# Kernel optimization log

Measured on AMD Instinct MI355X. Metric: run time of the kernel, lower is better.

## Reference

```python
import jax, jax.numpy as jnp
import numpy as np

E, H, I, R, T, TOPK = 8, 1024, 2816, 8, 4096, 2
SCALING = 2.0  # lora_alpha / r = 16 / 8


def setup_inputs() -> dict:
    key = jax.random.key(0)
    ks = jax.random.split(key, 12)
    inp = {
        "hidden_states": jax.random.normal(ks[0], (T, H), dtype=jnp.float32),
        "routing_weights": jax.random.uniform(ks[1], (T, TOPK), dtype=jnp.float32),
        "selected_experts": jax.random.randint(ks[2], (T, TOPK), 0, E),
        # frozen base expert weights, (G, K, N) layout
        "gate_proj": jax.random.normal(ks[3], (E, H, I), dtype=jnp.float32) * 0.02,
        "up_proj": jax.random.normal(ks[4], (E, H, I), dtype=jnp.float32) * 0.02,
        "down_proj": jax.random.normal(ks[5], (E, I, H), dtype=jnp.float32) * 0.02,
        # LoRA adapters, A: [E, in, r], B: [E, r, out]  (B random, not zero, so delta is exercised)
        "gate_A": jax.random.normal(ks[6], (E, H, R), dtype=jnp.float32) * 0.02,
        "gate_B": jax.random.normal(ks[7], (E, R, I), dtype=jnp.float32) * 0.02,
        "up_A": jax.random.normal(ks[8], (E, H, R), dtype=jnp.float32) * 0.02,
        "up_B": jax.random.normal(ks[9], (E, R, I), dtype=jnp.float32) * 0.02,
        "down_A": jax.random.normal(ks[10], (E, I, R), dtype=jnp.float32) * 0.02,
        "down_B": jax.random.normal(ks[11], (E, R, H), dtype=jnp.float32) * 0.02,
    }
    return inp


def _moe_lora_forward(x, routing_weights, selected_experts,
                      gate_proj, up_proj, down_proj,
                      gate_A, gate_B, up_A, up_B, down_A, down_B):
    # combine weights per (token, expert): [T, E]
    combine = jnp.sum(
        jax.nn.one_hot(selected_experts, E, dtype=x.dtype) * routing_weights[..., None],
        axis=1,
    )
    out = jnp.zeros_like(x)
    for e in range(E):  # static small loop over experts
        g = x @ gate_proj[e] + SCALING * ((x @ gate_A[e]) @ gate_B[e])
        u = x @ up_proj[e] + SCALING * ((x @ up_A[e]) @ up_B[e])
        h = jax.nn.silu(g) * u  # [T, I]
        y = h @ down_proj[e] + SCALING * ((h @ down_A[e]) @ down_B[e])  # [T, H]
        out = out + combine[:, e:e + 1] * y
    return out


def reference(hidden_states, routing_weights, selected_experts,
              gate_proj, up_proj, down_proj,
              gate_A, gate_B, up_A, up_B, down_A, down_B):
    return _moe_lora_forward(hidden_states, routing_weights, selected_experts,
                             gate_proj, up_proj, down_proj,
                             gate_A, gate_B, up_A, up_B, down_A, down_B)
```

## Files before the change

kernel.cpp:

```cpp
#include <hip/hip_runtime.h>
#include <stdint.h>

#define T_TOK 4096
#define NE 8
#define HH 1024
#define II 2816
#define HE 1056
#define IEW 2944
#define HT 23
#define RRK 8
#define NPAIR (T_TOK*2)
#define ROWCAP 10240
#define MT_MAX 40
#define SCAL 2.0f

typedef short v8s __attribute__((ext_vector_type(8)));
typedef float v4f __attribute__((ext_vector_type(4)));

__device__ __forceinline__ unsigned short f2bf(float f){
  union { float f; unsigned u; } c; c.f = f;
  unsigned u = c.u;
  u += 0x7FFFu + ((u >> 16) & 1u);
  return (unsigned short)(u >> 16);
}
__device__ __forceinline__ float bf2f(unsigned short h){
  union { unsigned u; float f; } c; c.u = ((unsigned)h) << 16;
  return c.f;
}
__device__ __forceinline__ void gload16(const void* g, void* l){
  __builtin_amdgcn_global_load_lds(
      (const __attribute__((address_space(1))) unsigned int*)g,
      (__attribute__((address_space(3))) unsigned int*)l, 16, 0, 0);
}
__device__ __forceinline__ void fence_(){ asm volatile("" ::: "memory"); }

__global__ void route_count(const int* __restrict__ sel, int* __restrict__ counts,
                            int* __restrict__ bases, int* __restrict__ tile_e,
                            int* __restrict__ tile_r0){
  __shared__ int c[NE];
  int tid = threadIdx.x;
  if (tid < NE) c[tid] = 0;
  __syncthreads();
  for (int p = tid; p < NPAIR; p += 256) atomicAdd(&c[sel[p]], 1);
  __syncthreads();
  if (tid == 0){
    int b = 0;
    for (int e = 0; e < NE; e++){ counts[e] = c[e]; bases[e] = b; b += ((c[e] + 255) >> 8) << 8; }
    bases[NE] = b;
    int t = 0;
    for (int e = 0; e < NE; e++){
      int nt = (c[e] + 255) >> 8;
      for (int i = 0; i < nt; i++){ tile_e[t] = e; tile_r0[t] = bases[e] + i * 256; t++; }
    }
    for (; t < MT_MAX; t++){ tile_e[t] = -1; tile_r0[t] = 0; }
  }
}

__global__ void route_fill(const int* __restrict__ sel, const float* __restrict__ rw,
                           const int* __restrict__ bases,
                           int* __restrict__ row_token, int* __restrict__ row_expert,
                           float* __restrict__ row_w, int* __restrict__ pair2row){
  int e = blockIdx.x;
  int lane = threadIdx.x;
  if (e == NE){
    for (int idx = bases[NE] + lane; idx < ROWCAP; idx += 64){
      row_token[idx] = -1; row_expert[idx] = 0; row_w[idx] = 0.f;
    }
    return;
  }
  int base = bases[e];
  int cnt = 0;
  for (int chunk = 0; chunk < NPAIR; chunk += 64){
    int p = chunk + lane;
    bool m = (sel[p] == e);
    unsigned long long mask = __ballot(m);
    if (m){
      int pos = __popcll(mask & ((1ull << lane) - 1ull));
      int dst = base + cnt + pos;
      row_token[dst] = p >> 1;
      row_expert[dst] = e;
      row_w[dst] = rw[p];
      pair2row[p] = dst;
    }
    cnt += __popcll(mask);
  }
  int nb = bases[e + 1];
  for (int idx = base + cnt + lane; idx < nb; idx += 64){
    row_token[idx] = -1; row_expert[idx] = e; row_w[idx] = 0.f;
  }
}

__global__ void transpose_cvt(const float* __restrict__ W, unsigned short* __restrict__ Wt,
                              int K, int N, int KE){
  int e = blockIdx.y;
  int tilesK = K >> 6;
  int kt = (blockIdx.x % tilesK) * 64;
  int nt = (blockIdx.x / tilesK) * 64;
  __shared__ float tile[64][65];
  int tid = threadIdx.x;
  int r = tid >> 2;
  int c0 = (tid & 3) * 16;
  const float* src = W + (size_t)e * K * N + (size_t)(kt + r) * N + nt + c0;
  #pragma unroll
  for (int i = 0; i < 4; i++){
    float4 v = *(const float4*)(src + i * 4);
    tile[r][c0 + i*4 + 0] = v.x; tile[r][c0 + i*4 + 1] = v.y;
    tile[r][c0 + i*4 + 2] = v.z; tile[r][c0 + i*4 + 3] = v.w;
  }
  __syncthreads();
  union { unsigned short us[16]; uint4 q[2]; } pk;
  #pragma unroll
  for (int j = 0; j < 16; j++) pk.us[j] = f2bf(tile[c0 + j][r]);
  unsigned short* dst = Wt + (size_t)e * N * KE + (size_t)(nt + r) * KE + kt + c0;
  *(uint4*)(dst) = pk.q[0];
  *(uint4*)(dst + 8) = pk.q[1];
}

__global__ void ext_fill_pair(unsigned short* __restrict__ Wtg, unsigned short* __restrict__ Wtu,
                              const float* __restrict__ gB, const float* __restrict__ uB){
  int idx = blockIdx.x * 256 + threadIdx.x;
  if (idx >= NE * II) return;
  int e = idx / II, n = idx % II;
  unsigned short* g = Wtg + ((size_t)e * II + n) * HE + HH;
  unsigned short* u = Wtu + ((size_t)e * II + n) * HE + HH;
  #pragma unroll
  for (int j = 0; j < 8; j++){
    g[j] = f2bf(gB[((size_t)e * RRK + j) * II + n]);
    u[j] = 0;
    g[8 + j] = 0;
    u[8 + j] = f2bf(uB[((size_t)e * RRK + j) * II + n]);
  }
  #pragma unroll
  for (int j = 16; j < 32; j++){ g[j] = 0; u[j] = 0; }
}

__global__ void ext_fill_down(unsigned short* __restrict__ Wtd, const float* __restrict__ dB){
  int idx = blockIdx.x * 256 + threadIdx.x;
  if (idx >= NE * HH) return;
  int e = idx / HH, n = idx % HH;
  unsigned short* d = Wtd + ((size_t)e * HH + n) * IEW + II;
  #pragma unroll
  for (int j = 0; j < 8; j++) d[j] = f2bf(dB[((size_t)e * RRK + j) * HH + n]);
  for (int j = 8; j < 128; j++) d[j] = 0;
}

__global__ void gxa_kernel(const float* __restrict__ x, const float* __restrict__ gA,
                           const float* __restrict__ uA, const int* __restrict__ row_token,
                           const int* __restrict__ row_expert,
                           unsigned short* __restrict__ Xg){
  int p = blockIdx.x; int tid = threadIdx.x;
  int tok = row_token[p]; int e = row_expert[p];
  int k0 = tid * 4;
  float4 xv = make_float4(0.f, 0.f, 0.f, 0.f);
  if (tok >= 0) xv = *(const float4*)(x + (size_t)tok * HH + k0);
  uint2 o;
  o.x = (unsigned)f2bf(xv.x) | ((unsigned)f2bf(xv.y) << 16);
  o.y = (unsigned)f2bf(xv.z) | ((unsigned)f2bf(xv.w) << 16);
  *(uint2*)(Xg + (size_t)p * HE + k0) = o;

  float ag[8], au[8];
  #pragma unroll
  for (int r = 0; r < 8; r++){ ag[r] = 0.f; au[r] = 0.f; }
  if (tok >= 0){
    const float* pg = gA + ((size_t)e * HH + k0) * RRK;
    const float* pu = uA + ((size_t)e * HH + k0) * RRK;
    float xs[4] = {xv.x, xv.y, xv.z, xv.w};
    #pragma unroll
    for (int j = 0; j < 4; j++){
      #pragma unroll
      for (int r = 0; r < 8; r++){
        ag[r] += xs[j] * pg[j * RRK + r];
        au[r] += xs[j] * pu[j * RRK + r];
      }
    }
  }
  __shared__ float redg[8][4], redu[8][4];
  int lane = tid & 63, wv = tid >> 6;
  #pragma unroll
  for (int r = 0; r < 8; r++){
    float v1 = ag[r], v2 = au[r];
    for (int off = 32; off > 0; off >>= 1){ v1 += __shfl_down(v1, off); v2 += __shfl_down(v2, off); }
    if (lane == 0){ redg[r][wv] = v1; redu[r][wv] = v2; }
  }
  __syncthreads();
  if (tid < 8)
    Xg[(size_t)p * HE + HH + tid] = f2bf(SCAL * (redg[tid][0] + redg[tid][1] + redg[tid][2] + redg[tid][3]));
  else if (tid < 16){
    int r = tid - 8;
    Xg[(size_t)p * HE + HH + 8 + r] = f2bf(SCAL * (redu[r][0] + redu[r][1] + redu[r][2] + redu[r][3]));
  } else if (tid < 32){
    Xg[(size_t)p * HE + HH + tid] = 0;
  }
}

__global__ void ha_kernel(const unsigned short* __restrict__ hbuf, const float* __restrict__ dA,
                          const int* __restrict__ row_expert, unsigned short* __restrict__ hout){
  int p = blockIdx.x; int tid = threadIdx.x;
  int e = row_expert[p];
  float a[8];
  #pragma unroll
  for (int r = 0; r < 8; r++) a[r] = 0.f;
  for (int i = 0; i < 11; i++){
    int k = i * 256 + tid;
    float hv = bf2f(hbuf[(size_t)(k >> 7) * (ROWCAP * 128) + (size_t)p * 128 + (k & 127)]);
    const float* pd = dA + ((size_t)e * II + k) * RRK;
    #pragma unroll
    for (int r = 0; r < 8; r++) a[r] += hv * pd[r];
  }
  __shared__ float red[8][4];
  int lane = tid & 63, wv = tid >> 6;
  #pragma unroll
  for (int r = 0; r < 8; r++){
    float v = a[r];
    for (int off = 32; off > 0; off >>= 1) v += __shfl_down(v, off);
    if (lane == 0) red[r][wv] = v;
  }
  __syncthreads();
  unsigned short* ext = hout + (size_t)22 * (ROWCAP * 128) + (size_t)p * 128;
  if (tid < 8)
    ext[tid] = f2bf(SCAL * (red[tid][0] + red[tid][1] + red[tid][2] + red[tid][3]));
  else if (tid < 128)
    ext[tid] = 0;
}

__launch_bounds__(512, 2)
__global__ void gemm1_kernel(const unsigned short* __restrict__ Xg,
                             const unsigned short* __restrict__ Wtg,
                             const unsigned short* __restrict__ Wtu,
                             const int* __restrict__ tile_e,
                             const int* __restrict__ tile_r0,
                             unsigned short* __restrict__ hbuf){
  int hw = blockIdx.x;
  int lg = (hw & 7) * 110 + (hw >> 3);
  int mt = lg / 22;
  int n0 = (lg % 22) * 128;

  int e = tile_e[mt];
  if (e < 0) return;
  int row0 = tile_r0[mt];

  __shared__ unsigned short lds[2][4 * 4096];
  int tid = threadIdx.x;
  int lane = tid & 63;
  int w = tid >> 6;
  int wm = w >> 1;
  int wn = w & 1;
  int g = lane >> 4, r16 = lane & 15;

  const unsigned short* srcA = Xg + (size_t)row0 * HE;
  const unsigned short* srcG = Wtg + ((size_t)e * II + n0) * HE;
  const unsigned short* srcU = Wtu + ((size_t)e * II + n0) * HE;

  v4f accg[4][4], accu[4][4];
  #pragma unroll
  for (int i = 0; i < 4; i++)
    #pragma unroll
    for (int j = 0; j < 4; j++){
      accg[i][j] = (v4f){0.f, 0.f, 0.f, 0.f};
      accu[i][j] = (v4f){0.f, 0.f, 0.f, 0.f};
    }

  int uA0 = tid, uA1 = tid + 512;
  int rA0 = uA0 >> 2, rA1 = uA1 >> 2;
  size_t gA0 = (size_t)rA0 * HE + ((uA0 & 3) ^ ((rA0 >> 1) & 3)) * 8;
  size_t gA1 = (size_t)rA1 * HE + ((uA1 & 3) ^ ((rA1 >> 1) & 3)) * 8;
  int lA0 = (uA0 & ~63) * 8, lA1 = (uA1 & ~63) * 8;
  int rB = tid >> 2;
  size_t gB = (size_t)rB * HE + ((tid & 3) ^ ((rB >> 1) & 3)) * 8;
  int lB = (tid & ~63) * 8;

  const int NT = HE / 32;

  {
    unsigned short* buf = lds[0];
    gload16(srcA + gA0, buf + lA0);
    gload16(srcA + gA1, buf + lA1);
    gload16(srcG + gB, buf + 8192 + lB);
    gload16(srcU + gB, buf + 12288 + lB);
  }

  for (int t = 0; t < NT; t++){
    if (t + 1 < NT){
      unsigned short* nbuf = lds[(t + 1) & 1];
      int ks = (t + 1) * 32;
      gload16(srcA + gA0 + ks, nbuf + lA0);
      gload16(srcA + gA1 + ks, nbuf + lA1);
      gload16(srcG + gB + ks, nbuf + 8192 + lB);
      gload16(srcU + gB + ks, nbuf + 12288 + lB);
      asm volatile("s_waitcnt vmcnt(4)" ::: "memory");
    } else {
      asm volatile("s_waitcnt vmcnt(0)" ::: "memory");
    }
    __builtin_amdgcn_s_barrier();
    fence_();
    const unsigned short* buf = lds[t & 1];
    v8s a[4], bg[4], bu[4];
    #pragma unroll
    for (int f = 0; f < 4; f++){
      int rowA = wm * 64 + f * 16 + r16;
      int ca = g ^ ((rowA >> 1) & 3);
      a[f] = *(const v8s*)(buf + rowA * 32 + ca * 8);
      int rowB = wn * 64 + f * 16 + r16;
      int cb = g ^ ((rowB >> 1) & 3);
      bg[f] = *(const v8s*)(buf + 8192 + rowB * 32 + cb * 8);
      bu[f] = *(const v8s*)(buf + 12288 + rowB * 32 + cb * 8);
    }
    #pragma unroll
    for (int fm = 0; fm < 4; fm++)
      #pragma unroll
      for (int fn = 0; fn < 4; fn++){
        accg[fm][fn] = __builtin_amdgcn_mfma_f32_16x16x32_bf16(a[fm], bg[fn], accg[fm][fn], 0, 0, 0);
        accu[fm][fn] = __builtin_amdgcn_mfma_f32_16x16x32_bf16(a[fm], bu[fn], accu[fm][fn], 0, 0, 0);
      }
    fence_();
    __builtin_amdgcn_s_barrier();
    fence_();
  }

  unsigned short* sh = (unsigned short*)lds;
  #pragma unroll
  for (int fm = 0; fm < 4; fm++)
    #pragma unroll
    for (int fn = 0; fn < 4; fn++)
      #pragma unroll
      for (int r = 0; r < 4; r++){
        int lrow = wm * 64 + fm * 16 + g * 4 + r;
        int lcol = wn * 64 + fn * 16 + r16;
        float gg = accg[fm][fn][r];
        float uu = accu[fm][fn][r];
        float hh = (gg / (1.f + __expf(-gg))) * uu;
        int ch = (lcol >> 3) ^ (lrow & 7);
        sh[lrow * 128 + ch * 8 + (lcol & 7)] = f2bf(hh);
      }
  __syncthreads();
  unsigned short* dst = hbuf + ((size_t)(n0 >> 7) * ROWCAP + row0) * 128;
  #pragma unroll
  for (int pass = 0; pass < 8; pass++){
    int idx2 = pass * 512 + tid;
    int row = idx2 >> 4;
    int ch = idx2 & 15;
    int chs = ch ^ (row & 7);
    v8s val = *(const v8s*)(sh + row * 128 + chs * 8);
    *(v8s*)(dst + row * 128 + ch * 8) = val;
  }
}

__launch_bounds__(512, 2)
__global__ void gemm2_kernel(const unsigned short* __restrict__ hbuf,
                             const unsigned short* __restrict__ Wtd,
                             const int* __restrict__ tile_e,
                             const int* __restrict__ tile_r0,
                             const float* __restrict__ row_w,
                             float* __restrict__ Y){
  int hw = blockIdx.x;
  int lg = (hw & 7) * 20 + (hw >> 3);
  int mt = lg / 4;
  int n0 = (lg % 4) * 256;

  int e = tile_e[mt];
  if (e < 0) return;
  int row0 = tile_r0[mt];

  __shared__ unsigned short lds[2][2 * 8192];
  int tid = threadIdx.x;
  int lane = tid & 63;
  int w = tid >> 6;
  int wm = w >> 1;
  int wn = w & 1;
  int g = lane >> 4, r16 = lane & 15;

  const unsigned short* srcA = hbuf + (size_t)row0 * 128;
  const unsigned short* srcB = Wtd + ((size_t)e * HH + n0) * IEW;

  v4f acc[4][8];
  #pragma unroll
  for (int i = 0; i < 4; i++)
    #pragma unroll
    for (int j = 0; j < 8; j++) acc[i][j] = (v4f){0.f, 0.f, 0.f, 0.f};

  int u0 = tid, u1 = tid + 512;
  int r0_ = u0 >> 2, r1_ = u1 >> 2;
  int c0_ = (u0 & 3) ^ ((r0_ >> 1) & 3), c1_ = (u1 & 3) ^ ((r1_ >> 1) & 3);
  size_t aoff0 = (size_t)r0_ * 128 + c0_ * 8;
  size_t aoff1 = (size_t)r1_ * 128 + c1_ * 8;
  size_t boff0 = (size_t)r0_ * IEW + c0_ * 8;
  size_t boff1 = (size_t)r1_ * IEW + c1_ * 8;
  int l0 = (u0 & ~63) * 8, l1 = (u1 & ~63) * 8;

  const int NT = IEW / 32;

  {
    unsigned short* buf = lds[0];
    gload16(srcA + aoff0, buf + l0);
    gload16(srcA + aoff1, buf + l1);
    gload16(srcB + boff0, buf + 8192 + l0);
    gload16(srcB + boff1, buf + 8192 + l1);
  }

  for (int t = 0; t < NT; t++){
    if (t + 1 < NT){
      unsigned short* nbuf = lds[(t + 1) & 1];
      int ks = (t + 1) * 32;
      size_t abase = (size_t)(ks >> 7) * (ROWCAP * 128) + (ks & 127);
      gload16(srcA + abase + aoff0, nbuf + l0);
      gload16(srcA + abase + aoff1, nbuf + l1);
      gload16(srcB + (size_t)ks + boff0, nbuf + 8192 + l0);
      gload16(srcB + (size_t)ks + boff1, nbuf + 8192 + l1);
      asm volatile("s_waitcnt vmcnt(4)" ::: "memory");
    } else {
      asm volatile("s_waitcnt vmcnt(0)" ::: "memory");
    }
    __builtin_amdgcn_s_barrier();
    fence_();
    const unsigned short* buf = lds[t & 1];
    v8s a[4], b[8];
    #pragma unroll
    for (int f = 0; f < 4; f++){
      int rowA = wm * 64 + f * 16 + r16;
      int ca = g ^ ((rowA >> 1) & 3);
      a[f] = *(const v8s*)(buf + rowA * 32 + ca * 8);
    }
    #pragma unroll
    for (int fn = 0; fn < 8; fn++){
      int rowB = wn * 128 + fn * 16 + r16;
      int cb = g ^ ((rowB >> 1) & 3);
      b[fn] = *(const v8s*)(buf + 8192 + rowB * 32 + cb * 8);
    }
    #pragma unroll
    for (int fm = 0; fm < 4; fm++)
      #pragma unroll
      for (int fn = 0; fn < 8; fn++)
        acc[fm][fn] = __builtin_amdgcn_mfma_f32_16x16x32_bf16(a[fm], b[fn], acc[fm][fn], 0, 0, 0);
    fence_();
    __builtin_amdgcn_s_barrier();
    fence_();
  }

  #pragma unroll
  for (int fm = 0; fm < 4; fm++){
    #pragma unroll
    for (int r = 0; r < 4; r++){
      int lrow = wm * 64 + fm * 16 + g * 4 + r;
      int grow = row0 + lrow;
      float wgt = row_w[grow];
      #pragma unroll
      for (int fn = 0; fn < 8; fn++){
        int lcol = wn * 128 + fn * 16 + r16;
        Y[(size_t)grow * HH + n0 + lcol] = wgt * acc[fm][fn][r];
      }
    }
  }
}

__global__ void combine_kernel(const float* __restrict__ Y, const int* __restrict__ pair2row,
                               float* __restrict__ out){
  int t = blockIdx.x;
  int c = threadIdx.x * 4;
  int r0 = pair2row[2 * t];
  int r1 = pair2row[2 * t + 1];
  float4 a = *(const float4*)(Y + (size_t)r0 * HH + c);
  float4 b = *(const float4*)(Y + (size_t)r1 * HH + c);
  float4 o = make_float4(a.x + b.x, a.y + b.y, a.z + b.z, a.w + b.w);
  *(float4*)(out + (size_t)t * HH + c) = o;
}

extern "C" void kernel_launch(void* const* d_in, const int* in_sizes, int n_in,
                              void* d_out, int out_size, void* d_ws, size_t ws_size,
                              hipStream_t stream){
  const float* x         = (const float*)d_in[0];
  const float* rw        = (const float*)d_in[1];
  const int*   sel       = (const int*)d_in[2];
  const float* gate_proj = (const float*)d_in[3];
  const float* up_proj   = (const float*)d_in[4];
  const float* down_proj = (const float*)d_in[5];
  const float* gate_A    = (const float*)d_in[6];
  const float* gate_B    = (const float*)d_in[7];
  const float* up_A      = (const float*)d_in[8];
  const float* up_B      = (const float*)d_in[9];
  const float* down_A    = (const float*)d_in[10];
  const float* down_B    = (const float*)d_in[11];
  float* out = (float*)d_out;
  char* ws = (char*)d_ws;

  constexpr size_t OFF_COUNTS = 0;
  constexpr size_t OFF_BASES  = 256;
  constexpr size_t OFF_TILE_E = 512;
  constexpr size_t OFF_TILE_R0 = 1024;
  constexpr size_t OFF_ROWTOK = 2048;
  constexpr size_t OFF_ROWEXP = OFF_ROWTOK + (size_t)ROWCAP * 4;
  constexpr size_t OFF_ROWW   = OFF_ROWEXP + (size_t)ROWCAP * 4;
  constexpr size_t OFF_P2R    = OFF_ROWW + (size_t)ROWCAP * 4;
  constexpr size_t OFF_XG     = OFF_P2R + (size_t)NPAIR * 4;
  constexpr size_t OFF_H      = OFF_XG + (size_t)ROWCAP * HE * 2;
  constexpr size_t OFF_WTG    = OFF_H + (size_t)HT * ROWCAP * 128 * 2;
  constexpr size_t OFF_WTU    = OFF_WTG + (size_t)NE * II * HE * 2;
  constexpr size_t OFF_WTD    = OFF_WTU + (size_t)NE * II * HE * 2;
  constexpr size_t OFF_Y      = OFF_WTG;

  int* counts    = (int*)(ws + OFF_COUNTS);
  int* bases     = (int*)(ws + OFF_BASES);
  int* tile_e    = (int*)(ws + OFF_TILE_E);
  int* tile_r0   = (int*)(ws + OFF_TILE_R0);
  int* row_token = (int*)(ws + OFF_ROWTOK);
  int* row_expert= (int*)(ws + OFF_ROWEXP);
  float* row_w   = (float*)(ws + OFF_ROWW);
  int* pair2row  = (int*)(ws + OFF_P2R);
  unsigned short* Xg   = (unsigned short*)(ws + OFF_XG);
  unsigned short* hbuf = (unsigned short*)(ws + OFF_H);
  unsigned short* Wtg  = (unsigned short*)(ws + OFF_WTG);
  unsigned short* Wtu  = (unsigned short*)(ws + OFF_WTU);
  unsigned short* Wtd  = (unsigned short*)(ws + OFF_WTD);
  float* Y = (float*)(ws + OFF_Y);

  route_count<<<1, 256, 0, stream>>>(sel, counts, bases, tile_e, tile_r0);
  route_fill<<<NE + 1, 64, 0, stream>>>(sel, rw, bases, row_token, row_expert, row_w, pair2row);
  transpose_cvt<<<dim3((HH >> 6) * (II >> 6), NE), 256, 0, stream>>>(gate_proj, Wtg, HH, II, HE);
  transpose_cvt<<<dim3((HH >> 6) * (II >> 6), NE), 256, 0, stream>>>(up_proj, Wtu, HH, II, HE);
  transpose_cvt<<<dim3((II >> 6) * (HH >> 6), NE), 256, 0, stream>>>(down_proj, Wtd, II, HH, IEW);
  ext_fill_pair<<<(NE * II + 255) / 256, 256, 0, stream>>>(Wtg, Wtu, gate_B, up_B);
  ext_fill_down<<<(NE * HH + 255) / 256, 256, 0, stream>>>(Wtd, down_B);
  gxa_kernel<<<ROWCAP, 256, 0, stream>>>(x, gate_A, up_A, row_token, row_expert, Xg);
  gemm1_kernel<<<MT_MAX * (II / 128), 512, 0, stream>>>(Xg, Wtg, Wtu, tile_e, tile_r0, hbuf);
  ha_kernel<<<ROWCAP, 256, 0, stream>>>(hbuf, down_A, row_expert, hbuf);
  gemm2_kernel<<<MT_MAX * (HH / 256), 512, 0, stream>>>(hbuf, Wtd, tile_e, tile_r0, row_w, Y);
  combine_kernel<<<T_TOK, 256, 0, stream>>>(Y, pair2row, out);
}
```

Measured before the change: 556.3 us.

## Split-K the down-projection GEMM into two halves, reduced in the combine kernel

The gemm2 grid is doubled so each block handles half of the K dimension (46 of 92 k-steps). Each half writes its partial result to a separate Y buffer, and combine_kernel now sums four partials per token instead of two. The goal is to fill more of the CUs, since the old grid launched only 160 blocks. The cost is twice as many fp32 Y writes and reads, plus a larger workspace region that reuses the space of the consumed gate/up weights.

```diff
diff --git a/kernel.cpp b/kernel.cpp
--- a/kernel.cpp
+++ b/kernel.cpp
@@ -351,11 +351,13 @@
                              const int* __restrict__ tile_e,
                              const int* __restrict__ tile_r0,
                              const float* __restrict__ row_w,
-                             float* __restrict__ Y){
+                             float* __restrict__ Y2){
   int hw = blockIdx.x;
-  int lg = (hw & 7) * 20 + (hw >> 3);
-  int mt = lg / 4;
-  int n0 = (lg % 4) * 256;
+  int lg = (hw & 7) * 40 + (hw >> 3);
+  int mt = lg >> 3;
+  int rem = lg & 7;
+  int n0 = (rem >> 1) * 256;
+  int half = rem & 1;
 
   int e = tile_e[mt];
   if (e < 0) return;
@@ -387,25 +389,24 @@
   size_t boff1 = (size_t)r1_ * IEW + c1_ * 8;
   int l0 = (u0 & ~63) * 8, l1 = (u1 & ~63) * 8;
 
-  const int NT = IEW / 32;
-
-  {
-    unsigned short* buf = lds[0];
-    gload16(srcA + aoff0, buf + l0);
-    gload16(srcA + aoff1, buf + l1);
-    gload16(srcB + boff0, buf + 8192 + l0);
-    gload16(srcB + boff1, buf + 8192 + l1);
-  }
-
-  for (int t = 0; t < NT; t++){
-    if (t + 1 < NT){
-      unsigned short* nbuf = lds[(t + 1) & 1];
-      int ks = (t + 1) * 32;
-      size_t abase = (size_t)(ks >> 7) * (ROWCAP * 128) + (ks & 127);
-      gload16(srcA + abase + aoff0, nbuf + l0);
-      gload16(srcA + abase + aoff1, nbuf + l1);
-      gload16(srcB + (size_t)ks + boff0, nbuf + 8192 + l0);
-      gload16(srcB + (size_t)ks + boff1, nbuf + 8192 + l1);
+  const int NHALF = (IEW / 32) / 2;
+  int tbeg = half * NHALF;
+  int tend = tbeg + NHALF;
+
+  auto stage = [&](int t, unsigned short* buf){
+    int ks = t * 32;
+    size_t abase = (size_t)(ks >> 7) * (ROWCAP * 128) + (ks & 127);
+    gload16(srcA + abase + aoff0, buf + l0);
+    gload16(srcA + abase + aoff1, buf + l1);
+    gload16(srcB + (size_t)ks + boff0, buf + 8192 + l0);
+    gload16(srcB + (size_t)ks + boff1, buf + 8192 + l1);
+  };
+
+  stage(tbeg, lds[tbeg & 1]);
+
+  for (int t = tbeg; t < tend; t++){
+    if (t + 1 < tend){
+      stage(t + 1, lds[(t + 1) & 1]);
       asm volatile("s_waitcnt vmcnt(4)" ::: "memory");
     } else {
       asm volatile("s_waitcnt vmcnt(0)" ::: "memory");
@@ -436,6 +437,7 @@
     fence_();
   }
 
+  float* Yh = Y2 + (size_t)half * ROWCAP * HH;
   #pragma unroll
   for (int fm = 0; fm < 4; fm++){
     #pragma unroll
@@ -446,21 +448,28 @@
       #pragma unroll
       for (int fn = 0; fn < 8; fn++){
         int lcol = wn * 128 + fn * 16 + r16;
-        Y[(size_t)grow * HH + n0 + lcol] = wgt * acc[fm][fn][r];
+        Yh[(size_t)grow * HH + n0 + lcol] = wgt * acc[fm][fn][r];
       }
     }
   }
 }
 
-__global__ void combine_kernel(const float* __restrict__ Y, const int* __restrict__ pair2row,
+__global__ void combine_kernel(const float* __restrict__ Y2, const int* __restrict__ pair2row,
                                float* __restrict__ out){
   int t = blockIdx.x;
   int c = threadIdx.x * 4;
   int r0 = pair2row[2 * t];
   int r1 = pair2row[2 * t + 1];
-  float4 a = *(const float4*)(Y + (size_t)r0 * HH + c);
-  float4 b = *(const float4*)(Y + (size_t)r1 * HH + c);
-  float4 o = make_float4(a.x + b.x, a.y + b.y, a.z + b.z, a.w + b.w);
+  const float* Y0 = Y2;
+  const float* Y1 = Y2 + (size_t)ROWCAP * HH;
+  float4 a0 = *(const float4*)(Y0 + (size_t)r0 * HH + c);
+  float4 a1 = *(const float4*)(Y1 + (size_t)r0 * HH + c);
+  float4 b0 = *(const float4*)(Y0 + (size_t)r1 * HH + c);
+  float4 b1 = *(const float4*)(Y1 + (size_t)r1 * HH + c);
+  float4 o = make_float4(a0.x + a1.x + b0.x + b1.x,
+                         a0.y + a1.y + b0.y + b1.y,
+                         a0.z + a1.z + b0.z + b1.z,
+                         a0.w + a1.w + b0.w + b1.w);
   *(float4*)(out + (size_t)t * HH + c) = o;
 }
 
@@ -510,7 +519,7 @@
   unsigned short* Wtg  = (unsigned short*)(ws + OFF_WTG);
   unsigned short* Wtu  = (unsigned short*)(ws + OFF_WTU);
   unsigned short* Wtd  = (unsigned short*)(ws + OFF_WTD);
-  float* Y = (float*)(ws + OFF_Y);
+  float* Y2 = (float*)(ws + OFF_Y);
 
   route_count<<<1, 256, 0, stream>>>(sel, counts, bases, tile_e, tile_r0);
   route_fill<<<NE + 1, 64, 0, stream>>>(sel, rw, bases, row_token, row_expert, row_w, pair2row);
@@ -522,6 +531,6 @@
   gxa_kernel<<<ROWCAP, 256, 0, stream>>>(x, gate_A, up_A, row_token, row_expert, Xg);
   gemm1_kernel<<<MT_MAX * (II / 128), 512, 0, stream>>>(Xg, Wtg, Wtu, tile_e, tile_r0, hbuf);
   ha_kernel<<<ROWCAP, 256, 0, stream>>>(hbuf, down_A, row_expert, hbuf);
-  gemm2_kernel<<<MT_MAX * (HH / 256), 512, 0, stream>>>(hbuf, Wtd, tile_e, tile_r0, row_w, Y);
-  combine_kernel<<<T_TOK, 256, 0, stream>>>(Y, pair2row, out);
-}
+  gemm2_kernel<<<MT_MAX * (HH / 256) * 2, 512, 0, stream>>>(hbuf, Wtd, tile_e, tile_r0, row_w, Y2);
+  combine_kernel<<<T_TOK, 256, 0, stream>>>(Y2, pair2row, out);
+}
```

Measured after the change: 559.5 us. No clear change (+0.6%).
